# Performance work log

Measured on AMD Instinct MI355X. Metric: run time of the kernel, lower is better.

The kernel has to match this reference:

```python
import jax, jax.numpy as jnp
import numpy as np

H = 2048  # hidden_size
B = 32    # hardcoded batch in module
T = 4     # sequence length per sample
F = 19    # LSTM input features


def setup_inputs() -> dict:
    key = jax.random.key(0)
    ks = jax.random.split(key, 14)
    s = 0.02
    def n(k, shape, scale=s):
        return jax.random.normal(k, shape, jnp.float32) * scale
    return {
        "state": jax.random.normal(ks[0], (B, T, 15), jnp.float32),
        "action": jax.random.normal(ks[1], (B, T, 4), jnp.float32),
        "conv_w": n(ks[2], (1,), 1.0),
        "conv_b": n(ks[3], (1,), 1.0),
        "w_ih0": n(ks[4], (4 * H, F)),
        "w_hh0": n(ks[5], (4 * H, H)),
        "b_ih0": n(ks[6], (4 * H,)),
        "b_hh0": n(ks[7], (4 * H,)),
        "w_ih1": n(ks[8], (4 * H, H)),
        "w_hh1": n(ks[9], (4 * H, H)),
        "b_ih1": n(ks[10], (4 * H,)),
        "b_hh1": n(ks[11], (4 * H,)),
        "lin_w": n(ks[12], (1, 4 * H)),
        "lin_b": n(ks[13], (1,)),
    }


def lstm_layer(x, w_ih, w_hh, b_ih, b_hh):
    # x: (T, B, in). PyTorch gate order: i, f, g, o. Zero initial state.
    Bn = x.shape[1]
    Hn = w_hh.shape[1]
    h0 = jnp.zeros((Bn, Hn), x.dtype)
    c0 = jnp.zeros((Bn, Hn), x.dtype)
    bias = b_ih + b_hh

    def step(carry, xt):
        h, c = carry
        g = xt @ w_ih.T + h @ w_hh.T + bias  # (B, 4H)
        i, f, gg, o = jnp.split(g, 4, axis=-1)
        c = jax.nn.sigmoid(f) * c + jax.nn.sigmoid(i) * jnp.tanh(gg)
        h = jax.nn.sigmoid(o) * jnp.tanh(c)
        return (h, c), h

    _, ys = jax.lax.scan(step, (h0, c0), x)
    return ys  # (T, B, H)


def reference(state, action, conv_w, conv_b, w_ih0, w_hh0, b_ih0, b_hh0,
              w_ih1, w_hh1, b_ih1, b_hh1, lin_w, lin_b):
    x = jnp.concatenate((state, action), axis=2)       # (B, T, 19)
    # Conv1d(1->1, k=1) on (T,1,19) is a scalar affine; tanh activation.
    x = jnp.tanh(conv_w[0] * x + conv_b[0])            # (B, T, 19)
    # Batch all 32 independent per-sample LSTM calls into one batched LSTM.
    x = jnp.transpose(x, (1, 0, 2))                    # (T, B, 19)
    h = lstm_layer(x, w_ih0, w_hh0, b_ih0, b_hh0)      # (T, B, H)
    h = lstm_layer(h, w_ih1, w_hh1, b_ih1, b_hh1)      # (T, B, H)
    h = jnp.transpose(h, (1, 0, 2)).reshape(B, T * H)  # (32, 4H) sample-major, matches torch reshape
    return jax.nn.sigmoid(h @ lin_w.T + lin_b)         # (32, 1)
```

## Files before the change

### kernel.cpp

```cpp
#include <hip/hip_runtime.h>
#include <hip/hip_bf16.h>
#include <math.h>

typedef __bf16 bf16_t;
typedef bf16_t bf16x8 __attribute__((ext_vector_type(8)));
typedef bf16_t bf16x4 __attribute__((ext_vector_type(4)));
typedef float  f32x4  __attribute__((ext_vector_type(4)));
typedef float  vf4    __attribute__((ext_vector_type(4)));

#define HH 2048
#define BB 32
#define TT 4
#define FF 19
#define NBLK 256
#define NTHR 512

#define LDS_WHH   0
#define LDS_X     131072
#define LDS_WIH0  141312
#define LDS_B0    143872
#define LDS_B1    144000
#define LDS_GP    144128
#define LDS_RED   152576
#define LDS_TOTAL 152608

#define WS_BCAST  8192
#define BAR_BYTES 12288
#define WS_H0     16384
#define WS_H1     540672
#define WS_G1     1064960

__device__ __forceinline__ float sigm(float x) { return 1.0f / (1.0f + expf(-x)); }

__device__ __forceinline__ void gbar_arrive(char* barbase, int slot, int blk) {
    __syncthreads();
    if (threadIdx.x == 0) {
        unsigned* base = (unsigned*)(barbase + slot * 1024);
        if (__hip_atomic_fetch_add(base + (blk & 7) * 16, 1u, __ATOMIC_RELAXED, __HIP_MEMORY_SCOPE_AGENT) == 31u)
            if (__hip_atomic_fetch_add(base + 128, 1u, __ATOMIC_RELAXED, __HIP_MEMORY_SCOPE_AGENT) == 7u) {
                unsigned* bc = (unsigned*)(barbase + WS_BCAST);
                #pragma unroll
                for (int g = 0; g < 8; ++g)
                    __hip_atomic_store(bc + g * 32, (unsigned)(slot + 1), __ATOMIC_RELAXED, __HIP_MEMORY_SCOPE_AGENT);
            }
    }
}
__device__ __forceinline__ void gbar_wait(char* barbase, int slot, int blk) {
    if (threadIdx.x == 0) {
        unsigned* line = (unsigned*)(barbase + WS_BCAST) + (blk & 7) * 32;
        while (__hip_atomic_load(line, __ATOMIC_RELAXED, __HIP_MEMORY_SCOPE_AGENT) < (unsigned)(slot + 1))
            __builtin_amdgcn_s_sleep(1);
    }
    __syncthreads();
}

__device__ __forceinline__ void load_w_lds(char* smem, const float* __restrict__ w, int blk, int tid) {
    char* dst = smem + LDS_WHH;
    #pragma unroll 1
    for (int base = 0; base < 32; base += 8) {
        vf4 v[8];
        #pragma unroll
        for (int j = 0; j < 8; ++j) {
            int row = base + j;
            int gr = (row >> 3) * 2048 + blk * 8 + (row & 7);
            v[j] = *reinterpret_cast<const vf4*>(w + (size_t)gr * 2048 + tid * 4);
        }
        #pragma unroll
        for (int j = 0; j < 8; ++j) {
            int row = base + j;
            bf16x4 bv;
            bv[0] = (bf16_t)v[j][0]; bv[1] = (bf16_t)v[j][1];
            bv[2] = (bf16_t)v[j][2]; bv[3] = (bf16_t)v[j][3];
            unsigned byte = (unsigned)(row * 4096) + (((unsigned)(tid * 8)) ^ (((unsigned)(row & 7)) << 4));
            *reinterpret_cast<bf16x4*>(dst + byte) = bv;
        }
    }
}

__device__ __forceinline__ void step_gemm(const __hip_bfloat16* __restrict__ hprev,
                                          const char* smem, float* gparts,
                                          int lane, int wv) {
    const int q  = wv >> 1;
    const int kh = wv & 1;
    const int mt = q >> 1, nt = q & 1;
    const int r = lane & 15, g4 = lane >> 4;
    f32x4 acc0 = {0.f,0.f,0.f,0.f}, acc1 = {0.f,0.f,0.f,0.f};
    const char* bbase = smem + LDS_WHH;
    const int n = nt * 16 + r;
    const unsigned brow = (unsigned)(n * 4096);
    const unsigned bsw = ((unsigned)(n & 7)) << 4;
    const __hip_bfloat16* aptr = hprev + (mt * 16 + r) * 2048 + g4 * 8;
    const int k0 = kh * 32;
    #pragma unroll
    for (int ks = 0; ks < 32; ks += 2) {
        int ka = k0 + ks, kb = k0 + ks + 1;
        bf16x8 a0 = *reinterpret_cast<const bf16x8*>(aptr + ka * 32);
        bf16x8 b0 = *reinterpret_cast<const bf16x8*>(bbase + brow + (((unsigned)(ka * 64 + g4 * 16)) ^ bsw));
        acc0 = __builtin_amdgcn_mfma_f32_16x16x32_bf16(a0, b0, acc0, 0, 0, 0);
        bf16x8 a1 = *reinterpret_cast<const bf16x8*>(aptr + kb * 32);
        bf16x8 b1 = *reinterpret_cast<const bf16x8*>(bbase + brow + (((unsigned)(kb * 64 + g4 * 16)) ^ bsw));
        acc1 = __builtin_amdgcn_mfma_f32_16x16x32_bf16(a1, b1, acc1, 0, 0, 0);
    }
    f32x4 s = acc0 + acc1;
    #pragma unroll
    for (int r2 = 0; r2 < 4; ++r2)
        gparts[(kh * 32 + mt * 16 + g4 * 4 + r2) * 33 + nt * 16 + r] = s[r2];
}

__device__ __forceinline__ void store_h(__hip_bfloat16* p, float x) {
    __hip_bfloat16 hv = __float2bfloat16(x);
    unsigned short bits = *reinterpret_cast<unsigned short*>(&hv);
    __hip_atomic_store((unsigned short*)p, bits, __ATOMIC_RELAXED, __HIP_MEMORY_SCOPE_AGENT);
}

__global__ __launch_bounds__(NTHR, 2) void fused_lstm(
    const float* __restrict__ state, const float* __restrict__ action,
    const float* __restrict__ conv_w, const float* __restrict__ conv_b,
    const float* __restrict__ w_ih0, const float* __restrict__ w_hh0,
    const float* __restrict__ b_ih0, const float* __restrict__ b_hh0,
    const float* __restrict__ w_ih1, const float* __restrict__ w_hh1,
    const float* __restrict__ b_ih1, const float* __restrict__ b_hh1,
    const float* __restrict__ lin_w, const float* __restrict__ lin_b,
    float* __restrict__ out, char* __restrict__ ws)
{
    extern __shared__ char smem[];
    float* x_lds    = (float*)(smem + LDS_X);
    float* wih0_lds = (float*)(smem + LDS_WIH0);
    float* b0_lds   = (float*)(smem + LDS_B0);
    float* b1_lds   = (float*)(smem + LDS_B1);
    float* gparts   = (float*)(smem + LDS_GP);
    float* red      = (float*)(smem + LDS_RED);

    const int tid  = threadIdx.x;
    const int blk  = blockIdx.x;
    const int lane = tid & 63;
    const int wv   = tid >> 6;
    const int m    = tid >> 3;
    const int u    = tid & 7;

    __hip_bfloat16* h0_ws = (__hip_bfloat16*)(ws + WS_H0);
    __hip_bfloat16* h1_ws = (__hip_bfloat16*)(ws + WS_H1);
    float*          g1    = (float*)(ws + WS_G1);

    {
        float cw = conv_w[0], cb = conv_b[0];
        for (int i = tid; i < TT * BB * FF; i += NTHR) {
            int f = i % FF; int tb = i / FF; int t = tb >> 5; int mm = tb & 31;
            float v = (f < 15) ? state[(mm * TT + t) * 15 + f] : action[(mm * TT + t) * 4 + (f - 15)];
            x_lds[tb * 20 + f] = tanhf(cw * v + cb);
        }
        for (int i = tid; i < 32 * FF; i += NTHR) {
            int n = i / FF; int f = i % FF;
            int gr = (n >> 3) * 2048 + blk * 8 + (n & 7);
            wih0_lds[n * 20 + f] = w_ih0[(size_t)gr * FF + f];
        }
        if (tid < 32) {
            int gr = (tid >> 3) * 2048 + blk * 8 + (tid & 7);
            b0_lds[tid] = b_ih0[gr] + b_hh0[gr];
        }
    }
    __syncthreads();

    float c0 = 0.f;
    if (tid < 256) {
        float gv[4];
        #pragma unroll
        for (int gate = 0; gate < 4; ++gate) {
            int n = gate * 8 + u;
            float a = b0_lds[n];
            const float* xr = &x_lds[m * 20];
            const float* wr = &wih0_lds[n * 20];
            #pragma unroll
            for (int f = 0; f < FF; ++f) a += xr[f] * wr[f];
            gv[gate] = a;
        }
        float ig = sigm(gv[0]), fg = sigm(gv[1]), g2 = tanhf(gv[2]), og = sigm(gv[3]);
        c0 = fg * c0 + ig * g2;
        store_h(h0_ws + (size_t)m * 2048 + blk * 8 + u, og * tanhf(c0));
    }
    gbar_arrive(ws, 0, blk);
    load_w_lds(smem, w_hh0, blk, tid);
    gbar_wait(ws, 0, blk);

    for (int t = 1; t < TT; ++t) {
        step_gemm(h0_ws + (size_t)(t - 1) * BB * HH, smem, gparts, lane, wv);
        __syncthreads();
        if (tid < 256) {
            float gv[4];
            #pragma unroll
            for (int gate = 0; gate < 4; ++gate) {
                int n = gate * 8 + u;
                float a = gparts[m * 33 + n] + gparts[(32 + m) * 33 + n] + b0_lds[n];
                const float* xr = &x_lds[(t * 32 + m) * 20];
                const float* wr = &wih0_lds[n * 20];
                #pragma unroll
                for (int f = 0; f < FF; ++f) a += xr[f] * wr[f];
                gv[gate] = a;
            }
            float ig = sigm(gv[0]), fg = sigm(gv[1]), g2 = tanhf(gv[2]), og = sigm(gv[3]);
            c0 = fg * c0 + ig * g2;
            store_h(h0_ws + (size_t)(t * 32 + m) * 2048 + blk * 8 + u, og * tanhf(c0));
        }
        gbar_arrive(ws, t, blk);
        if (t == 3) {
            load_w_lds(smem, w_ih1, blk, tid);
            if (tid < 32) {
                int gr = (tid >> 3) * 2048 + blk * 8 + (tid & 7);
                b1_lds[tid] = b_ih1[gr] + b_hh1[gr];
            }
        }
        gbar_wait(ws, t, blk);
    }

    {
        const int r = lane & 15, g4 = lane >> 4;
        const char* bbase = smem + LDS_WHH;
        const unsigned bsw0 = ((unsigned)(r & 7)) << 4;
        const int mt = wv;
        f32x4 acc0 = {0.f,0.f,0.f,0.f}, acc1 = {0.f,0.f,0.f,0.f};
        const __hip_bfloat16* aptr = h0_ws + (size_t)(mt * 16 + r) * 2048 + g4 * 8;
        #pragma unroll 4
        for (int ks = 0; ks < 64; ++ks) {
            bf16x8 a  = *reinterpret_cast<const bf16x8*>(aptr + ks * 32);
            bf16x8 b0 = *reinterpret_cast<const bf16x8*>(bbase + (unsigned)(r * 4096)        + (((unsigned)(ks * 64 + g4 * 16)) ^ bsw0));
            bf16x8 b1 = *reinterpret_cast<const bf16x8*>(bbase + (unsigned)((16 + r) * 4096) + (((unsigned)(ks * 64 + g4 * 16)) ^ bsw0));
            acc0 = __builtin_amdgcn_mfma_f32_16x16x32_bf16(a, b0, acc0, 0, 0, 0);
            acc1 = __builtin_amdgcn_mfma_f32_16x16x32_bf16(a, b1, acc1, 0, 0, 0);
        }
        #pragma unroll
        for (int r2 = 0; r2 < 4; ++r2) {
            int tb = mt * 16 + g4 * 4 + r2;
            g1[((size_t)tb * 256 + blk) * 32 + r]      = acc0[r2] + b1_lds[r];
            g1[((size_t)tb * 256 + blk) * 32 + 16 + r] = acc1[r2] + b1_lds[16 + r];
        }
    }
    __syncthreads();

    float c1 = 0.f;
    if (tid < 256) {
        float gv[4];
        #pragma unroll
        for (int gate = 0; gate < 4; ++gate) {
            int n = gate * 8 + u;
            gv[gate] = g1[((size_t)m * 256 + blk) * 32 + n];
        }
        float ig = sigm(gv[0]), fg = sigm(gv[1]), g2 = tanhf(gv[2]), og = sigm(gv[3]);
        c1 = fg * c1 + ig * g2;
        store_h(h1_ws + (size_t)m * 2048 + blk * 8 + u, og * tanhf(c1));
    }
    gbar_arrive(ws, 4, blk);
    load_w_lds(smem, w_hh1, blk, tid);
    gbar_wait(ws, 4, blk);

    for (int t = 1; t < TT; ++t) {
        step_gemm(h1_ws + (size_t)(t - 1) * BB * HH, smem, gparts, lane, wv);
        __syncthreads();
        if (tid < 256) {
            float gv[4];
            #pragma unroll
            for (int gate = 0; gate < 4; ++gate) {
                int n = gate * 8 + u;
                gv[gate] = gparts[m * 33 + n] + gparts[(32 + m) * 33 + n]
                         + g1[((size_t)(t * 32 + m) * 256 + blk) * 32 + n];
            }
            float ig = sigm(gv[0]), fg = sigm(gv[1]), g2 = tanhf(gv[2]), og = sigm(gv[3]);
            c1 = fg * c1 + ig * g2;
            store_h(h1_ws + (size_t)(t * 32 + m) * 2048 + blk * 8 + u, og * tanhf(c1));
        }
        gbar_arrive(ws, 4 + t, blk);
        gbar_wait(ws, 4 + t, blk);
    }

    if (blk < BB) {
        float part = 0.f;
        for (int i = tid; i < 1024; i += NTHR) {
            int k = i * 8; int t = k >> 11; int uu = k & 2047;
            uint4 hv = *reinterpret_cast<const uint4*>(h1_ws + (size_t)(t * 32 + blk) * 2048 + uu);
            const float* lw = lin_w + k;
            #pragma unroll
            for (int j = 0; j < 4; ++j) {
                unsigned wj = (&hv.x)[j];
                float lo = __uint_as_float(wj << 16);
                float hi = __uint_as_float(wj & 0xffff0000u);
                part += lo * lw[2 * j] + hi * lw[2 * j + 1];
            }
        }
        #pragma unroll
        for (int off = 32; off; off >>= 1) part += __shfl_down(part, off, 64);
        if (lane == 0) red[wv] = part;
        __syncthreads();
        if (tid == 0) {
            float s = red[0] + red[1] + red[2] + red[3] + red[4] + red[5] + red[6] + red[7] + lin_b[0];
            out[blk] = 1.f / (1.f + expf(-s));
        }
    }
}

extern "C" void kernel_launch(void* const* d_in, const int* in_sizes, int n_in,
                              void* d_out, int out_size, void* d_ws, size_t ws_size,
                              hipStream_t stream) {
    const float* state  = (const float*)d_in[0];
    const float* action = (const float*)d_in[1];
    const float* conv_w = (const float*)d_in[2];
    const float* conv_b = (const float*)d_in[3];
    const float* w_ih0  = (const float*)d_in[4];
    const float* w_hh0  = (const float*)d_in[5];
    const float* b_ih0  = (const float*)d_in[6];
    const float* b_hh0  = (const float*)d_in[7];
    const float* w_ih1  = (const float*)d_in[8];
    const float* w_hh1  = (const float*)d_in[9];
    const float* b_ih1  = (const float*)d_in[10];
    const float* b_hh1  = (const float*)d_in[11];
    const float* lin_w  = (const float*)d_in[12];
    const float* lin_b  = (const float*)d_in[13];
    float* out = (float*)d_out;
    char*  ws  = (char*)d_ws;

    hipMemsetAsync(ws, 0, BAR_BYTES, stream);

    hipLaunchKernelGGL(fused_lstm, dim3(NBLK), dim3(NTHR), LDS_TOTAL, stream,
                       state, action, conv_w, conv_b, w_ih0, w_hh0, b_ih0, b_hh0,
                       w_ih1, w_hh1, b_ih1, b_hh1, lin_w, lin_b, out, ws);
}
```

Measured before the change: 292.7 us.

## Prefetch layer-1 weights into registers across steps and fuse final linear

The layer-1 input weights are now loaded from global memory in slices during the layer-0 timesteps and held as bf16 in registers. The recurrent layer-1 weights are prefetched while the input-projection GEMM runs, so the LDS writes after each barrier no longer wait on global loads. The final linear layer is folded into the last LSTM steps: each block accumulates h·lin_w partials and combines them with global atomics plus a completion counter, which removes the last grid barrier and the separate reduction. This costs many extra registers, which risks spills or lower occupancy, and it relies on the facc and fcnt workspace being zeroed beforehand.

```diff
diff --git a/kernel.cpp b/kernel.cpp
--- a/kernel.cpp
+++ b/kernel.cpp
@@ -21,10 +21,11 @@
 #define LDS_B0    143872
 #define LDS_B1    144000
 #define LDS_GP    144128
-#define LDS_RED   152576
 #define LDS_TOTAL 152608
 
 #define WS_BCAST  8192
+#define WS_FACC   9216
+#define WS_FCNT   9600
 #define BAR_BYTES 12288
 #define WS_H0     16384
 #define WS_H1     540672
@@ -74,6 +75,15 @@
             unsigned byte = (unsigned)(row * 4096) + (((unsigned)(tid * 8)) ^ (((unsigned)(row & 7)) << 4));
             *reinterpret_cast<bf16x4*>(dst + byte) = bv;
         }
+    }
+}
+
+__device__ __forceinline__ void ds_write_pay(char* smem, const bf16x4* pay, int tid) {
+    char* dst = smem + LDS_WHH;
+    #pragma unroll
+    for (int row = 0; row < 32; ++row) {
+        unsigned byte = (unsigned)(row * 4096) + (((unsigned)(tid * 8)) ^ (((unsigned)(row & 7)) << 4));
+        *reinterpret_cast<bf16x4*>(dst + byte) = pay[row];
     }
 }
 
@@ -129,7 +139,6 @@
     float* b0_lds   = (float*)(smem + LDS_B0);
     float* b1_lds   = (float*)(smem + LDS_B1);
     float* gparts   = (float*)(smem + LDS_GP);
-    float* red      = (float*)(smem + LDS_RED);
 
     const int tid  = threadIdx.x;
     const int blk  = blockIdx.x;
@@ -141,7 +150,12 @@
     __hip_bfloat16* h0_ws = (__hip_bfloat16*)(ws + WS_H0);
     __hip_bfloat16* h1_ws = (__hip_bfloat16*)(ws + WS_H1);
     float*          g1    = (float*)(ws + WS_G1);
-
+    float*          facc  = (float*)(ws + WS_FACC);
+    unsigned*       fcnt  = (unsigned*)(ws + WS_FCNT);
+
+    bf16x4 pay[32];
+
+    float lw0 = 0.f, lw1 = 0.f, lw2 = 0.f, lw3 = 0.f, linb = 0.f;
     {
         float cw = conv_w[0], cb = conv_b[0];
         for (int i = tid; i < TT * BB * FF; i += NTHR) {
@@ -158,6 +172,12 @@
             int gr = (tid >> 3) * 2048 + blk * 8 + (tid & 7);
             b0_lds[tid] = b_ih0[gr] + b_hh0[gr];
         }
+        if (tid < 256) {
+            int col = blk * 8 + u;
+            lw0 = lin_w[col]; lw1 = lin_w[2048 + col];
+            lw2 = lin_w[4096 + col]; lw3 = lin_w[6144 + col];
+            linb = lin_b[0];
+        }
     }
     __syncthreads();
 
@@ -182,6 +202,7 @@
     load_w_lds(smem, w_hh0, blk, tid);
     gbar_wait(ws, 0, blk);
 
+    #pragma unroll
     for (int t = 1; t < TT; ++t) {
         step_gemm(h0_ws + (size_t)(t - 1) * BB * HH, smem, gparts, lane, wv);
         __syncthreads();
@@ -202,8 +223,23 @@
             store_h(h0_ws + (size_t)(t * 32 + m) * 2048 + blk * 8 + u, og * tanhf(c0));
         }
         gbar_arrive(ws, t, blk);
+        {
+            const int r0 = (t == 1) ? 0 : (t == 2) ? 10 : 21;
+            const int r1 = (t == 1) ? 10 : (t == 2) ? 21 : 32;
+            #pragma unroll
+            for (int row = 0; row < 32; ++row) {
+                if (row >= r0 && row < r1) {
+                    int gr = (row >> 3) * 2048 + blk * 8 + (row & 7);
+                    vf4 v = *reinterpret_cast<const vf4*>(w_ih1 + (size_t)gr * 2048 + tid * 4);
+                    bf16x4 bv;
+                    bv[0] = (bf16_t)v[0]; bv[1] = (bf16_t)v[1];
+                    bv[2] = (bf16_t)v[2]; bv[3] = (bf16_t)v[3];
+                    pay[row] = bv;
+                }
+            }
+        }
         if (t == 3) {
-            load_w_lds(smem, w_ih1, blk, tid);
+            ds_write_pay(smem, pay, tid);
             if (tid < 32) {
                 int gr = (tid >> 3) * 2048 + blk * 8 + (tid & 7);
                 b1_lds[tid] = b_ih1[gr] + b_hh1[gr];
@@ -219,13 +255,27 @@
         const int mt = wv;
         f32x4 acc0 = {0.f,0.f,0.f,0.f}, acc1 = {0.f,0.f,0.f,0.f};
         const __hip_bfloat16* aptr = h0_ws + (size_t)(mt * 16 + r) * 2048 + g4 * 8;
-        #pragma unroll 4
-        for (int ks = 0; ks < 64; ++ks) {
-            bf16x8 a  = *reinterpret_cast<const bf16x8*>(aptr + ks * 32);
-            bf16x8 b0 = *reinterpret_cast<const bf16x8*>(bbase + (unsigned)(r * 4096)        + (((unsigned)(ks * 64 + g4 * 16)) ^ bsw0));
-            bf16x8 b1 = *reinterpret_cast<const bf16x8*>(bbase + (unsigned)((16 + r) * 4096) + (((unsigned)(ks * 64 + g4 * 16)) ^ bsw0));
-            acc0 = __builtin_amdgcn_mfma_f32_16x16x32_bf16(a, b0, acc0, 0, 0, 0);
-            acc1 = __builtin_amdgcn_mfma_f32_16x16x32_bf16(a, b1, acc1, 0, 0, 0);
+        #pragma unroll
+        for (int c = 0; c < 4; ++c) {
+            #pragma unroll
+            for (int j = 0; j < 8; ++j) {
+                int row = c * 8 + j;
+                int gr = (row >> 3) * 2048 + blk * 8 + (row & 7);
+                vf4 v = *reinterpret_cast<const vf4*>(w_hh1 + (size_t)gr * 2048 + tid * 4);
+                bf16x4 bv;
+                bv[0] = (bf16_t)v[0]; bv[1] = (bf16_t)v[1];
+                bv[2] = (bf16_t)v[2]; bv[3] = (bf16_t)v[3];
+                pay[row] = bv;
+            }
+            #pragma unroll
+            for (int kk = 0; kk < 16; ++kk) {
+                int ks = c * 16 + kk;
+                bf16x8 a  = *reinterpret_cast<const bf16x8*>(aptr + ks * 32);
+                bf16x8 b0 = *reinterpret_cast<const bf16x8*>(bbase + (unsigned)(r * 4096)        + (((unsigned)(ks * 64 + g4 * 16)) ^ bsw0));
+                bf16x8 b1 = *reinterpret_cast<const bf16x8*>(bbase + (unsigned)((16 + r) * 4096) + (((unsigned)(ks * 64 + g4 * 16)) ^ bsw0));
+                acc0 = __builtin_amdgcn_mfma_f32_16x16x32_bf16(a, b0, acc0, 0, 0, 0);
+                acc1 = __builtin_amdgcn_mfma_f32_16x16x32_bf16(a, b1, acc1, 0, 0, 0);
+            }
         }
         #pragma unroll
         for (int r2 = 0; r2 < 4; ++r2) {
@@ -236,7 +286,7 @@
     }
     __syncthreads();
 
-    float c1 = 0.f;
+    float c1 = 0.f, fsum = 0.f;
     if (tid < 256) {
         float gv[4];
         #pragma unroll
@@ -246,12 +296,15 @@
         }
         float ig = sigm(gv[0]), fg = sigm(gv[1]), g2 = tanhf(gv[2]), og = sigm(gv[3]);
         c1 = fg * c1 + ig * g2;
-        store_h(h1_ws + (size_t)m * 2048 + blk * 8 + u, og * tanhf(c1));
+        float hval = og * tanhf(c1);
+        fsum += hval * lw0;
+        store_h(h1_ws + (size_t)m * 2048 + blk * 8 + u, hval);
     }
     gbar_arrive(ws, 4, blk);
-    load_w_lds(smem, w_hh1, blk, tid);
+    ds_write_pay(smem, pay, tid);
     gbar_wait(ws, 4, blk);
 
+    #pragma unroll
     for (int t = 1; t < TT; ++t) {
         step_gemm(h1_ws + (size_t)(t - 1) * BB * HH, smem, gparts, lane, wv);
         __syncthreads();
@@ -265,33 +318,29 @@
             }
             float ig = sigm(gv[0]), fg = sigm(gv[1]), g2 = tanhf(gv[2]), og = sigm(gv[3]);
             c1 = fg * c1 + ig * g2;
-            store_h(h1_ws + (size_t)(t * 32 + m) * 2048 + blk * 8 + u, og * tanhf(c1));
-        }
-        gbar_arrive(ws, 4 + t, blk);
-        gbar_wait(ws, 4 + t, blk);
-    }
-
-    if (blk < BB) {
-        float part = 0.f;
-        for (int i = tid; i < 1024; i += NTHR) {
-            int k = i * 8; int t = k >> 11; int uu = k & 2047;
-            uint4 hv = *reinterpret_cast<const uint4*>(h1_ws + (size_t)(t * 32 + blk) * 2048 + uu);
-            const float* lw = lin_w + k;
-            #pragma unroll
-            for (int j = 0; j < 4; ++j) {
-                unsigned wj = (&hv.x)[j];
-                float lo = __uint_as_float(wj << 16);
-                float hi = __uint_as_float(wj & 0xffff0000u);
-                part += lo * lw[2 * j] + hi * lw[2 * j + 1];
-            }
-        }
-        #pragma unroll
-        for (int off = 32; off; off >>= 1) part += __shfl_down(part, off, 64);
-        if (lane == 0) red[wv] = part;
-        __syncthreads();
-        if (tid == 0) {
-            float s = red[0] + red[1] + red[2] + red[3] + red[4] + red[5] + red[6] + red[7] + lin_b[0];
-            out[blk] = 1.f / (1.f + expf(-s));
+            float hval = og * tanhf(c1);
+            fsum += hval * ((t == 1) ? lw1 : (t == 2) ? lw2 : lw3);
+            if (t < 3) store_h(h1_ws + (size_t)(t * 32 + m) * 2048 + blk * 8 + u, hval);
+        }
+        if (t < 3) {
+            gbar_arrive(ws, 4 + t, blk);
+            gbar_wait(ws, 4 + t, blk);
+        }
+    }
+
+    if (tid < 256) {
+        float v = fsum;
+        v += __shfl_down(v, 4, 8);
+        v += __shfl_down(v, 2, 8);
+        v += __shfl_down(v, 1, 8);
+        if (u == 0) {
+            atomicAdd(facc + m, v);
+            asm volatile("s_waitcnt vmcnt(0)" ::: "memory");
+            unsigned old = __hip_atomic_fetch_add(fcnt + m, 1u, __ATOMIC_RELAXED, __HIP_MEMORY_SCOPE_AGENT);
+            if (old == (unsigned)(NBLK - 1)) {
+                float s = __hip_atomic_load(facc + m, __ATOMIC_RELAXED, __HIP_MEMORY_SCOPE_AGENT);
+                out[m] = 1.f / (1.f + expf(-(s + linb)));
+            }
         }
     }
 }
```

Measured after the change: 320.5 us. +9.5%, slower.
